# Kernel optimization log

Measured on AMD Instinct MI355X. Metric: run time of the kernel, lower is better.

Reference implementation:

```python
import jax, jax.numpy as jnp
import numpy as np

B, S, T = 4, 512, 512
V, D, F, H, DK, N = 32000, 512, 2048, 8, 64, 6
PAD = 0

# sinusoidal positional encoding table, matching the torch source exactly
_pos = np.arange(max(S, T))[:, None]
_i = np.arange(D // 2)[None, :]
_ang = _pos / (10000.0 ** (2 * _i / D))
_pe = np.empty((max(S, T), D), dtype=np.float32)
_pe[:, 0::2] = np.sin(_ang)
_pe[:, 1::2] = np.cos(_ang)
PE = jnp.asarray(_pe)


def setup_inputs() -> dict:
    key = jax.random.key(0)
    ks = iter(jax.random.split(key, 64))
    s = 0.02
    w = lambda shape: jax.random.normal(next(ks), shape, jnp.float32) * s
    inp = {
        'src': jax.random.randint(next(ks), (B, S), 0, V, jnp.int32),
        'trg': jax.random.randint(next(ks), (B, T), 0, V, jnp.int32),
        'emb_src': w((V, D)).at[PAD].set(0.0),
        'emb_trg': w((V, D)).at[PAD].set(0.0),
        # encoder stacks (leading axis = layer)
        'enc_wq': w((N, D, H * DK)), 'enc_wk': w((N, D, H * DK)),
        'enc_wv': w((N, D, H * DK)), 'enc_wo': w((N, H * DK, D)),
        'enc_ln1_g': jnp.ones((N, D)), 'enc_ln1_b': jnp.zeros((N, D)),
        'enc_w1': w((N, D, F)), 'enc_b1': jnp.zeros((N, F)),
        'enc_w2': w((N, F, D)), 'enc_b2': jnp.zeros((N, D)),
        'enc_ln2_g': jnp.ones((N, D)), 'enc_ln2_b': jnp.zeros((N, D)),
        # decoder stacks
        'dec_wq': w((N, D, H * DK)), 'dec_wk': w((N, D, H * DK)),
        'dec_wv': w((N, D, H * DK)), 'dec_wo': w((N, H * DK, D)),
        'dec_ln1_g': jnp.ones((N, D)), 'dec_ln1_b': jnp.zeros((N, D)),
        'dec_cq': w((N, D, H * DK)), 'dec_ck': w((N, D, H * DK)),
        'dec_cv': w((N, D, H * DK)), 'dec_co': w((N, H * DK, D)),
        'dec_ln2_g': jnp.ones((N, D)), 'dec_ln2_b': jnp.zeros((N, D)),
        'dec_w1': w((N, D, F)), 'dec_b1': jnp.zeros((N, F)),
        'dec_w2': w((N, F, D)), 'dec_b2': jnp.zeros((N, D)),
        'dec_ln3_g': jnp.ones((N, D)), 'dec_ln3_b': jnp.zeros((N, D)),
        'proj': w((D, V)),
    }
    return inp


def _ln(x, g, b, eps=1e-5):
    m = x.mean(-1, keepdims=True)
    v = ((x - m) ** 2).mean(-1, keepdims=True)
    return (x - m) * jax.lax.rsqrt(v + eps) * g + b


def _mha(xq, xkv, wq, wk, wv, wo, mask):
    b, lq, _ = xq.shape
    lk = xkv.shape[1]
    q = (xq @ wq).reshape(b, lq, H, DK).transpose(0, 2, 1, 3)   # bhqd
    k = (xkv @ wk).reshape(b, lk, H, DK).transpose(0, 2, 1, 3)  # bhkd
    v = (xkv @ wv).reshape(b, lk, H, DK).transpose(0, 2, 1, 3)  # bhkd
    scores = jnp.einsum('bhqd,bhkd->bhqk', q, k)
    scores = jnp.where(mask, -jnp.inf, scores)
    attn = jax.nn.softmax(scores * (DK ** -0.5), axis=-1)
    out = jnp.einsum('bhqk,bhkd->bhqd', attn, v)
    out = out.transpose(0, 2, 1, 3).reshape(b, lq, H * DK)
    return out @ wo


def _ffn(x, w1, b1, w2, b2):
    return jax.nn.relu(x @ w1 + b1) @ w2 + b2


def reference(src, trg, emb_src, emb_trg,
              enc_wq, enc_wk, enc_wv, enc_wo, enc_ln1_g, enc_ln1_b,
              enc_w1, enc_b1, enc_w2, enc_b2, enc_ln2_g, enc_ln2_b,
              dec_wq, dec_wk, dec_wv, dec_wo, dec_ln1_g, dec_ln1_b,
              dec_cq, dec_ck, dec_cv, dec_co, dec_ln2_g, dec_ln2_b,
              dec_w1, dec_b1, dec_w2, dec_b2, dec_ln3_g, dec_ln3_b,
              proj):
    scale = D ** 0.5
    src_pad = (src == PAD)[:, None, None, :]                 # [B,1,1,S]
    trg_pad = (trg == PAD)[:, None, None, :]                 # [B,1,1,T]
    causal = jnp.triu(jnp.ones((T, T), bool), 1)[None, None]  # [1,1,T,T]
    trg_mask = trg_pad | causal

    # encoder (dropout = identity in eval)
    x = emb_src[src] * scale + PE[None, :S]

    def enc_step(h, p):
        wq, wk, wv, wo, g1, b1, w1, bb1, w2, bb2, g2, b2 = p
        h = _ln(h + _mha(h, h, wq, wk, wv, wo, src_pad), g1, b1)
        h = _ln(h + _ffn(h, w1, bb1, w2, bb2), g2, b2)
        return h, None

    x_enc, _ = jax.lax.scan(enc_step, x,
        (enc_wq, enc_wk, enc_wv, enc_wo, enc_ln1_g, enc_ln1_b,
         enc_w1, enc_b1, enc_w2, enc_b2, enc_ln2_g, enc_ln2_b))

    # decoder
    y = emb_trg[trg] * scale + PE[None, :T]

    def dec_step(h, p):
        (wq, wk, wv, wo, g1, b1, cq, ck, cv, co, g2, b2,
         w1, bb1, w2, bb2, g3, b3) = p
        h = _ln(h + _mha(h, h, wq, wk, wv, wo, trg_mask), g1, b1)
        h = _ln(h + _mha(h, x_enc, cq, ck, cv, co, src_pad), g2, b2)
        h = _ln(h + _ffn(h, w1, bb1, w2, bb2), g3, b3)
        return h, None

    y, _ = jax.lax.scan(dec_step, y,
        (dec_wq, dec_wk, dec_wv, dec_wo, dec_ln1_g, dec_ln1_b,
         dec_cq, dec_ck, dec_cv, dec_co, dec_ln2_g, dec_ln2_b,
         dec_w1, dec_b1, dec_w2, dec_b2, dec_ln3_g, dec_ln3_b))

    return y @ proj  # [B, T, trg_vocab]
```

## Files before the change

### kernel.cpp

```cpp
#include <hip/hip_runtime.h>
#include <math.h>

#define BBATCH 4
#define SS 512
#define DDIM 512
#define FFN 2048
#define NHEAD 8
#define DHEAD 64
#define NL 6
#define NVOC 32000
#define MTOK (BBATCH*SS)
#define PAD_ID 0

typedef unsigned short u16;
typedef __attribute__((ext_vector_type(8))) short short8;
typedef __attribute__((ext_vector_type(4))) float f32x4;

__device__ __forceinline__ u16 f2bf(float f) {
    union { float f; unsigned u; } v; v.f = f;
    unsigned r = ((v.u >> 16) & 1u) + 0x7fffu;
    return (u16)((v.u + r) >> 16);
}

__device__ __forceinline__ void gload16(const u16* g, u16* l) {
    __builtin_amdgcn_global_load_lds(
        (const __attribute__((address_space(1))) void*)g,
        (__attribute__((address_space(3))) void*)l, 16, 0, 0);
}

template<int BM, int BN, int OUTBF, int RELU, int BIAS>
__device__ __forceinline__ void gemm_core(
    u16* __restrict__ AsB, u16* __restrict__ BsB,
    const u16* __restrict__ A, int lda,
    const u16* __restrict__ B, int ldb,
    void* __restrict__ Cv, int ldc,
    int row0, int col0, int K, const float* __restrict__ bias)
{
    const int tid  = threadIdx.x;
    const int lane = tid & 63;
    const int wid  = tid >> 6;
    const int wr   = wid >> 1, wc = wid & 1;
    constexpr int MF = BM / 32, NF = BN / 32, RA = BM / 64, RB = BN / 64;

    const u16* aSrc[RA]; int aOff[RA];
    #pragma unroll
    for (int r = 0; r < RA; r++) {
        int row = (tid >> 2) + r * 64;
        int slot = ((tid & 3) << 4) ^ ((row & 3) << 4);
        aSrc[r] = A + (size_t)(row0 + row) * lda + (slot >> 1);
        aOff[r] = r * 2048 + tid * 8;
    }
    const u16* bSrc[RB]; int bOff[RB];
    #pragma unroll
    for (int r = 0; r < RB; r++) {
        int row = (tid >> 2) + r * 64;
        int slot = ((tid & 3) << 4) ^ ((row & 3) << 4);
        bSrc[r] = B + (size_t)(col0 + row) * ldb + (slot >> 1);
        bOff[r] = r * 2048 + tid * 8;
    }

    f32x4 acc[MF][NF];
    const f32x4 zero = {0.f, 0.f, 0.f, 0.f};
    #pragma unroll
    for (int m = 0; m < MF; m++)
        #pragma unroll
        for (int n = 0; n < NF; n++) acc[m][n] = zero;

    const int nt = K / 32;
    #pragma unroll
    for (int r = 0; r < RA; r++) gload16(aSrc[r], AsB + aOff[r]);
    #pragma unroll
    for (int r = 0; r < RB; r++) gload16(bSrc[r], BsB + bOff[r]);
    __syncthreads();

    for (int t = 0; t < nt; t++) {
        const int cur = t & 1;
        if (t + 1 < nt) {
            u16* ad = AsB + (cur ^ 1) * (BM * 32);
            u16* bd = BsB + (cur ^ 1) * (BN * 32);
            #pragma unroll
            for (int r = 0; r < RA; r++) gload16(aSrc[r] + (t + 1) * 32, ad + aOff[r]);
            #pragma unroll
            for (int r = 0; r < RB; r++) gload16(bSrc[r] + (t + 1) * 32, bd + bOff[r]);
        }
        const u16* as = AsB + cur * (BM * 32);
        const u16* bs = BsB + cur * (BN * 32);
        short8 af[MF], bf[NF];
        #pragma unroll
        for (int m = 0; m < MF; m++) {
            int row = wr * (BM / 2) + m * 16 + (lane & 15);
            int slot = ((lane >> 4) << 4) ^ ((row & 3) << 4);
            af[m] = *(const short8*)&as[row * 32 + (slot >> 1)];
        }
        #pragma unroll
        for (int n = 0; n < NF; n++) {
            int row = wc * (BN / 2) + n * 16 + (lane & 15);
            int slot = ((lane >> 4) << 4) ^ ((row & 3) << 4);
            bf[n] = *(const short8*)&bs[row * 32 + (slot >> 1)];
        }
        #pragma unroll
        for (int m = 0; m < MF; m++)
            #pragma unroll
            for (int n = 0; n < NF; n++)
                acc[m][n] = __builtin_amdgcn_mfma_f32_16x16x32_bf16(af[m], bf[n], acc[m][n], 0, 0, 0);
        __syncthreads();
    }

    const int crow = row0 + wr * (BM / 2);
    const int ccol = col0 + wc * (BN / 2);
    #pragma unroll
    for (int m = 0; m < MF; m++) {
        #pragma unroll
        for (int n = 0; n < NF; n++) {
            int col = ccol + n * 16 + (lane & 15);
            float bv = BIAS ? bias[col] : 0.0f;
            #pragma unroll
            for (int i = 0; i < 4; i++) {
                int row = crow + m * 16 + ((lane >> 4) << 2) + i;
                float v = acc[m][n][i] + bv;
                if (RELU) v = fmaxf(v, 0.0f);
                if (OUTBF) ((u16*)Cv)[(size_t)row * ldc + col] = f2bf(v);
                else       ((float*)Cv)[(size_t)row * ldc + col] = v;
            }
        }
    }
}

template<int BM, int BN, int OUTBF, int RELU, int BIAS, int SWZ = 0>
__global__ __launch_bounds__(256) void mgemm(
    const u16* __restrict__ A, int lda, size_t aSb, size_t aSh,
    const u16* __restrict__ B, int ldb, size_t bSb, size_t bSh,
    void* __restrict__ Cv, int ldc, size_t cSb, size_t cSh,
    int K, const float* __restrict__ bias)
{
    __shared__ __align__(16) u16 As[2 * BM * 32];
    __shared__ __align__(16) u16 Bs[2 * BN * 32];
    int bx = blockIdx.x, by = blockIdx.y;
    if (SWZ) {
        int nwg = gridDim.x * gridDim.y;
        int lin = by * gridDim.x + bx;
        int cpx = nwg >> 3;
        int s = (lin & 7) * cpx + (lin >> 3);
        bx = s % gridDim.x; by = s / gridDim.x;
    }
    const int zb = blockIdx.z >> 3, zh = blockIdx.z & 7;
    const u16* Ab = A + (size_t)zb * aSb + (size_t)zh * aSh;
    const u16* Bb = B + (size_t)zb * bSb + (size_t)zh * bSh;
    void* Cb = OUTBF ? (void*)((u16*)Cv + (size_t)zb * cSb + (size_t)zh * cSh)
                     : (void*)((float*)Cv + (size_t)zb * cSb + (size_t)zh * cSh);
    gemm_core<BM, BN, OUTBF, RELU, BIAS>(As, Bs, Ab, lda, Bb, ldb, Cb, ldc,
                                          by * BM, bx * BN, K, bias);
}

template<int BM, int BN>
__global__ __launch_bounds__(256) void mgemm_dual(
    const u16* __restrict__ A1, int lda1, const u16* __restrict__ B1, int ldb1,
    u16* __restrict__ C1, int ldc1, int nx1, int nblk1,
    const u16* __restrict__ A2, int lda2, const u16* __restrict__ B2, int ldb2,
    u16* __restrict__ C2, int ldc2, int nx2,
    int K)
{
    __shared__ __align__(16) u16 As[2 * BM * 32];
    __shared__ __align__(16) u16 Bs[2 * BN * 32];
    int id = blockIdx.x;
    if (id < nblk1) {
        gemm_core<BM, BN, 1, 0, 0>(As, Bs, A1, lda1, B1, ldb1, C1, ldc1,
                                    (id / nx1) * BM, (id % nx1) * BN, K, nullptr);
    } else {
        id -= nblk1;
        gemm_core<BM, BN, 1, 0, 0>(As, Bs, A2, lda2, B2, ldb2, C2, ldc2,
                                    (id / nx2) * BM, (id % nx2) * BN, K, nullptr);
    }
}

template<int CAUSAL>
__global__ __launch_bounds__(256) void flash_attn(
    const u16* __restrict__ Qp, int ldq,
    const u16* __restrict__ Kp, int ldk,
    const u16* __restrict__ Vtp,
    u16* __restrict__ O,
    const int* __restrict__ ids)
{
    __shared__ __align__(16) u16 Kl[2][64 * 64];
    __shared__ __align__(16) u16 Vl[2][64 * 64];
    __shared__ __align__(16) u16 Pl[4][16 * 64];
    __shared__ float msk[SS];

    const int tid = threadIdx.x, lane = tid & 63, wid = tid >> 6;
    const int bh = blockIdx.y, b = bh >> 3, h = bh & 7;
    const int q0 = blockIdx.x * 64;

    for (int i = tid; i < SS; i += 256)
        msk[i] = (ids[b * SS + i] == PAD_ID) ? -1e30f : 0.0f;

    const int qloc = wid * 16 + (lane & 15);
    const u16* Qb = Qp + (size_t)(b * SS + q0 + qloc) * ldq + h * 64 + ((lane >> 4) * 8);
    short8 qf[2];
    qf[0] = *(const short8*)(Qb);
    qf[1] = *(const short8*)(Qb + 32);

    const u16* Kb = Kp + (size_t)b * SS * ldk + h * 64;
    const u16* Vb = Vtp + (size_t)(h * 64) * MTOK + b * SS;

    auto stage = [&](int buf, int kt) {
        int row = tid >> 3;
        int sl  = tid & 7;
        #pragma unroll
        for (int r = 0; r < 2; r++) {
            int rr = row + r * 32;
            int ls = sl ^ (rr & 7);
            gload16(Kb + (size_t)(kt * 64 + rr) * ldk + ls * 8, &Kl[buf][rr * 64 + sl * 8]);
            gload16(Vb + (size_t)rr * MTOK + kt * 64 + ls * 8, &Vl[buf][rr * 64 + sl * 8]);
        }
    };

    const int nt = CAUSAL ? (blockIdx.x + 1) : (SS / 64);
    stage(0, 0);
    __syncthreads();

    float m_i[4], l_i[4];
    f32x4 o_acc[4];
    const f32x4 zero = {0.f, 0.f, 0.f, 0.f};
    #pragma unroll
    for (int i = 0; i < 4; i++) { m_i[i] = -1e30f; l_i[i] = 0.0f; }
    #pragma unroll
    for (int n = 0; n < 4; n++) o_acc[n] = zero;

    for (int kt = 0; kt < nt; kt++) {
        int cur = kt & 1;
        if (kt + 1 < nt) stage(cur ^ 1, kt + 1);

        f32x4 s_acc[4];
        #pragma unroll
        for (int n = 0; n < 4; n++) s_acc[n] = zero;
        #pragma unroll
        for (int kk = 0; kk < 2; kk++) {
            #pragma unroll
            for (int n = 0; n < 4; n++) {
                int row = n * 16 + (lane & 15);
                int ls = (kk * 4 + (lane >> 4)) ^ (row & 7);
                short8 kf = *(const short8*)&Kl[cur][row * 64 + ls * 8];
                s_acc[n] = __builtin_amdgcn_mfma_f32_16x16x32_bf16(qf[kk], kf, s_acc[n], 0, 0, 0);
            }
        }

        float sv[4][4];
        #pragma unroll
        for (int n = 0; n < 4; n++) {
            int kg = kt * 64 + n * 16 + (lane & 15);
            float mk = msk[kg];
            #pragma unroll
            for (int i = 0; i < 4; i++) {
                float s = s_acc[n][i] * 0.125f + mk;
                if (CAUSAL) {
                    int qg = q0 + wid * 16 + ((lane >> 4) << 2) + i;
                    if (kg > qg) s = -1e30f;
                }
                sv[n][i] = s;
            }
        }
        float pm[4], mn[4], rs[4], ps[4];
        #pragma unroll
        for (int i = 0; i < 4; i++)
            pm[i] = fmaxf(fmaxf(sv[0][i], sv[1][i]), fmaxf(sv[2][i], sv[3][i]));
        #pragma unroll
        for (int i = 0; i < 4; i++) {
            #pragma unroll
            for (int msh = 1; msh <= 8; msh <<= 1)
                pm[i] = fmaxf(pm[i], __shfl_xor(pm[i], msh));
            mn[i] = fmaxf(m_i[i], pm[i]);
            rs[i] = __expf(m_i[i] - mn[i]);
            m_i[i] = mn[i];
        }
        float p[4][4];
        #pragma unroll
        for (int n = 0; n < 4; n++)
            #pragma unroll
            for (int i = 0; i < 4; i++)
                p[n][i] = (sv[n][i] < -1e29f) ? 0.0f : __expf(sv[n][i] - mn[i]);
        #pragma unroll
        for (int i = 0; i < 4; i++) {
            ps[i] = p[0][i] + p[1][i] + p[2][i] + p[3][i];
            #pragma unroll
            for (int msh = 1; msh <= 8; msh <<= 1)
                ps[i] += __shfl_xor(ps[i], msh);
            l_i[i] = l_i[i] * rs[i] + ps[i];
        }
        #pragma unroll
        for (int n = 0; n < 4; n++)
            #pragma unroll
            for (int i = 0; i < 4; i++)
                o_acc[n][i] *= rs[i];

        #pragma unroll
        for (int n = 0; n < 4; n++) {
            int k = n * 16 + (lane & 15);
            #pragma unroll
            for (int i = 0; i < 4; i++) {
                int q = ((lane >> 4) << 2) + i;
                Pl[wid][q * 64 + (((k >> 3) ^ (q & 7)) << 3) + (k & 7)] = f2bf(p[n][i]);
            }
        }
        asm volatile("s_waitcnt lgkmcnt(0)" ::: "memory");

        #pragma unroll
        for (int kk = 0; kk < 2; kk++) {
            int qrow = lane & 15;
            int lsp = (kk * 4 + (lane >> 4)) ^ (qrow & 7);
            short8 pa = *(const short8*)&Pl[wid][qrow * 64 + lsp * 8];
            #pragma unroll
            for (int nf = 0; nf < 4; nf++) {
                int row = nf * 16 + (lane & 15);
                int vs = (kk * 4 + (lane >> 4)) ^ (row & 7);
                short8 vf = *(const short8*)&Vl[cur][row * 64 + vs * 8];
                o_acc[nf] = __builtin_amdgcn_mfma_f32_16x16x32_bf16(pa, vf, o_acc[nf], 0, 0, 0);
            }
        }
        __syncthreads();
    }

    #pragma unroll
    for (int nf = 0; nf < 4; nf++) {
        int d = h * 64 + nf * 16 + (lane & 15);
        #pragma unroll
        for (int i = 0; i < 4; i++) {
            int qg = b * SS + q0 + wid * 16 + ((lane >> 4) << 2) + i;
            O[(size_t)qg * DDIM + d] = f2bf(o_acc[nf][i] / l_i[i]);
        }
    }
}

__device__ __forceinline__ void transp_core(const float* __restrict__ src, u16* __restrict__ dst,
                                            int N, int K, int n0, int k0)
{
    __shared__ u16 t[64][65];
    const int tid = threadIdx.x;
    #pragma unroll
    for (int i = 0; i < 16; i++) {
        int idx = tid + i * 256;
        int kr = idx >> 6, nc = idx & 63;
        t[kr][nc] = f2bf(src[(size_t)(k0 + kr) * N + n0 + nc]);
    }
    __syncthreads();
    #pragma unroll
    for (int i = 0; i < 16; i++) {
        int idx = tid + i * 256;
        int nr = idx >> 6, kc = idx & 63;
        dst[(size_t)(n0 + nr) * K + k0 + kc] = t[kc][nr];
    }
}

__global__ __launch_bounds__(256) void transp(const float* __restrict__ src, u16* __restrict__ dst,
                                              int N, int K, size_t sStride, size_t dStride)
{
    transp_core(src + (size_t)blockIdx.z * sStride, dst + (size_t)blockIdx.z * dStride,
                N, K, blockIdx.x * 64, blockIdx.y * 64);
}

#define OFF_QK 0u
#define OFF_WV 524288u
#define OFF_WO 786432u
#define OFF_CQ 1048576u
#define OFF_CK 1310720u
#define OFF_CV 1572864u
#define OFF_CO 1835008u
#define OFF_W1 2097152u
#define OFF_W2 3145728u
#define WBLK   4194304u
#define M2CNT  262144u
#define MF1CNT 1048576u

__global__ __launch_bounds__(256) void transpW(
    const float* p0, const float* p1, const float* p2, const float* p3,
    const float* p4, const float* p5, const float* p6, const float* p7,
    const float* p8, const float* p9, const float* p10, const float* p11,
    u16* __restrict__ wreg)
{
    int z = blockIdx.z;
    int w = z % 12, l = z / 12;
    const float* ptrs[12] = {p0,p1,p2,p3,p4,p5,p6,p7,p8,p9,p10,p11};
    const float* src = ptrs[w] + (size_t)l * M2CNT;
    u16* dst = wreg + (w < 4 ? (size_t)l * WBLK + (size_t)w * M2CNT
                             : (size_t)(NL + l) * WBLK + (size_t)(w - 4) * M2CNT);
    transp_core(src, dst, 512, 512, blockIdx.x * 64, blockIdx.y * 64);
}

__global__ __launch_bounds__(256) void transpF1(const float* __restrict__ e,
                                                const float* __restrict__ d, u16* __restrict__ wreg)
{
    int z = blockIdx.z; int l = z % NL, w = z / NL;
    const float* src = (w ? d : e) + (size_t)l * MF1CNT;
    u16* dst = wreg + (size_t)(w * NL + l) * WBLK + OFF_W1;
    transp_core(src, dst, 2048, 512, blockIdx.x * 64, blockIdx.y * 64);
}

__global__ __launch_bounds__(256) void transpF2(const float* __restrict__ e,
                                                const float* __restrict__ d, u16* __restrict__ wreg)
{
    int z = blockIdx.z; int l = z % NL, w = z / NL;
    const float* src = (w ? d : e) + (size_t)l * MF1CNT;
    u16* dst = wreg + (size_t)(w * NL + l) * WBLK + OFF_W2;
    transp_core(src, dst, 512, 2048, blockIdx.x * 64, blockIdx.y * 64);
}

__global__ void pe_kernel(float* __restrict__ PEt)
{
    int pos = blockIdx.x, d = threadIdx.x;
    int i = d >> 1;
    double freq = exp(-(2.0 * (double)i / (double)DDIM) * log(10000.0));
    double ang = (double)pos * freq;
    PEt[pos * DDIM + d] = (float)((d & 1) ? cos(ang) : sin(ang));
}

__global__ void embed_kernel(const int* __restrict__ ids, const float* __restrict__ emb,
                             const float* __restrict__ PEt,
                             float* __restrict__ out, u16* __restrict__ outb)
{
    int tok = blockIdx.x;
    int d = threadIdx.x;
    int pos = tok & (SS - 1);
    int id = ids[tok];
    float val = emb[(size_t)id * DDIM + d] * 22.62741699796952f + PEt[pos * DDIM + d];
    out[(size_t)tok * DDIM + d] = val;
    outb[(size_t)tok * DDIM + d] = f2bf(val);
}

__global__ __launch_bounds__(256) void add_ln_kernel(float* __restrict__ x,
    const float* __restrict__ addv, const float* __restrict__ g,
    const float* __restrict__ bta, u16* __restrict__ xb)
{
    int row = blockIdx.x;
    int tid = threadIdx.x;
    size_t base = (size_t)row * DDIM;
    __shared__ float sbuf[4];

    float v0 = x[base + tid]       + addv[base + tid];
    float v1 = x[base + tid + 256] + addv[base + tid + 256];

    float s = v0 + v1;
    #pragma unroll
    for (int o = 32; o > 0; o >>= 1) s += __shfl_down(s, o);
    if ((tid & 63) == 0) sbuf[tid >> 6] = s;
    __syncthreads();
    float mean = (sbuf[0] + sbuf[1] + sbuf[2] + sbuf[3]) * (1.0f / DDIM);
    __syncthreads();

    float d0 = v0 - mean, d1 = v1 - mean;
    float ss = d0 * d0 + d1 * d1;
    #pragma unroll
    for (int o = 32; o > 0; o >>= 1) ss += __shfl_down(ss, o);
    if ((tid & 63) == 0) sbuf[tid >> 6] = ss;
    __syncthreads();
    float var = (sbuf[0] + sbuf[1] + sbuf[2] + sbuf[3]) * (1.0f / DDIM);
    float inv = rsqrtf(var + 1e-5f);

    float o0 = d0 * inv * g[tid]       + bta[tid];
    float o1 = d1 * inv * g[tid + 256] + bta[tid + 256];
    x[base + tid] = o0;
    x[base + tid + 256] = o1;
    xb[base + tid] = f2bf(o0);
    xb[base + tid + 256] = f2bf(o1);
}

extern "C" void kernel_launch(void* const* d_in, const int* in_sizes, int n_in,
                              void* d_out, int out_size, void* d_ws, size_t ws_size,
                              hipStream_t stream)
{
    (void)in_sizes; (void)n_in; (void)out_size;

    const int*   src      = (const int*)  d_in[0];
    const int*   trg      = (const int*)  d_in[1];
    const float* emb_src  = (const float*)d_in[2];
    const float* emb_trg  = (const float*)d_in[3];
    const float* enc_wq   = (const float*)d_in[4];
    const float* enc_wk   = (const float*)d_in[5];
    const float* enc_wv   = (const float*)d_in[6];
    const float* enc_wo   = (const float*)d_in[7];
    const float* enc_ln1g = (const float*)d_in[8];
    const float* enc_ln1b = (const float*)d_in[9];
    const float* enc_w1   = (const float*)d_in[10];
    const float* enc_b1   = (const float*)d_in[11];
    const float* enc_w2   = (const float*)d_in[12];
    const float* enc_b2   = (const float*)d_in[13];
    const float* enc_ln2g = (const float*)d_in[14];
    const float* enc_ln2b = (const float*)d_in[15];
    const float* dec_wq   = (const float*)d_in[16];
    const float* dec_wk   = (const float*)d_in[17];
    const float* dec_wv   = (const float*)d_in[18];
    const float* dec_wo   = (const float*)d_in[19];
    const float* dec_ln1g = (const float*)d_in[20];
    const float* dec_ln1b = (const float*)d_in[21];
    const float* dec_cq   = (const float*)d_in[22];
    const float* dec_ck   = (const float*)d_in[23];
    const float* dec_cv   = (const float*)d_in[24];
    const float* dec_co   = (const float*)d_in[25];
    const float* dec_ln2g = (const float*)d_in[26];
    const float* dec_ln2b = (const float*)d_in[27];
    const float* dec_w1   = (const float*)d_in[28];
    const float* dec_b1   = (const float*)d_in[29];
    const float* dec_w2   = (const float*)d_in[30];
    const float* dec_b2   = (const float*)d_in[31];
    const float* dec_ln3g = (const float*)d_in[32];
    const float* dec_ln3b = (const float*)d_in[33];
    const float* proj     = (const float*)d_in[34];

    float* OUT = (float*)d_out;
    char* base = (char*)d_ws;

    const size_t MSZ = (size_t)MTOK * DDIM;
    size_t off = 0;
    auto carve = [&](size_t bytes) { char* p = base + off; off += (bytes + 255) & ~(size_t)255; return p; };

    float* X      = (float*)carve(MSZ * 4);
    float* Yb     = (float*)carve(MSZ * 4);
    float* T1     = (float*)carve(MSZ * 4);
    u16*   Xb     = (u16*)  carve(MSZ * 2);
    u16*   Ybf    = (u16*)  carve(MSZ * 2);
    u16*   QKb    = (u16*)  carve((size_t)MTOK * 1024 * 2);
    u16*   Vt     = (u16*)  carve((size_t)512 * MTOK * 2);
    u16*   CTX    = (u16*)  carve(MSZ * 2);
    u16*   HFF    = (u16*)  carve((size_t)MTOK * FFN * 2);
    u16*   Kcr    = (u16*)  carve((size_t)NL * MTOK * 512 * 2);
    u16*   Vtc    = (u16*)  carve((size_t)NL * 512 * MTOK * 2);
    u16*   projT  = (u16*)  carve((size_t)NVOC * 512 * 2);
    float* PEt    = (float*)carve((size_t)SS * DDIM * 4);

    const size_t WFULL_B = (size_t)12 * WBLK * 2;
    bool full = (ws_size >= off + WFULL_B);
    u16* Wreg = (u16*)carve(full ? WFULL_B : (size_t)WBLK * 2);

    auto T = [&](const float* s, u16* d, int Kd, int Nd, size_t ss, size_t ds, int L) {
        transp<<<dim3(Nd / 64, Kd / 64, L), 256, 0, stream>>>(s, d, Nd, Kd, ss, ds);
    };

    pe_kernel<<<SS, DDIM, 0, stream>>>(PEt);
    T(proj, projT, 512, NVOC, 0, 0, 1);
    if (full) {
        transpW<<<dim3(8, 8, 12 * NL), 256, 0, stream>>>(
            enc_wq, enc_wk, enc_wv, enc_wo,
            dec_wq, dec_wk, dec_wv, dec_wo,
            dec_cq, dec_ck, dec_cv, dec_co, Wreg);
        transpF1<<<dim3(32, 8, 2 * NL), 256, 0, stream>>>(enc_w1, dec_w1, Wreg);
        transpF2<<<dim3(8, 32, 2 * NL), 256, 0, stream>>>(enc_w2, dec_w2, Wreg);
    }

    auto self_attn = [&](const u16* xsrc, const u16* wb, const int* mask_ids, int causal) {
        mgemm_dual<64, 128><<<dim3(384), 256, 0, stream>>>(
            xsrc, 512, wb + OFF_QK, 512, QKb, 1024, 8, 256,
            wb + OFF_WV, 512, xsrc, 512, Vt, MTOK, 16,
            512);
        if (causal)
            flash_attn<1><<<dim3(8, 32), 256, 0, stream>>>(QKb, 1024, QKb + 512, 1024, Vt, CTX, mask_ids);
        else
            flash_attn<0><<<dim3(8, 32), 256, 0, stream>>>(QKb, 1024, QKb + 512, 1024, Vt, CTX, mask_ids);
        mgemm<64, 64, 0, 0, 0><<<dim3(8, 32, 1), 256, 0, stream>>>(
            CTX, 512, 0, 0, wb + OFF_WO, 512, 0, 0, T1, 512, 0, 0, 512, nullptr);
    };

    const size_t M2 = M2CNT, MF1 = MF1CNT;

    embed_kernel<<<MTOK, DDIM, 0, stream>>>(src, emb_src, PEt, X, Xb);
    for (int l = 0; l < NL; l++) {
        u16* wb;
        if (full) wb = Wreg + (size_t)l * WBLK;
        else {
            wb = Wreg;
            T(enc_wq + l * M2,  wb + OFF_QK,          512, 512,  0, 0, 1);
            T(enc_wk + l * M2,  wb + OFF_QK + M2,     512, 512,  0, 0, 1);
            T(enc_wv + l * M2,  wb + OFF_WV,          512, 512,  0, 0, 1);
            T(enc_wo + l * M2,  wb + OFF_WO,          512, 512,  0, 0, 1);
            T(enc_w1 + l * MF1, wb + OFF_W1,          512, 2048, 0, 0, 1);
            T(enc_w2 + l * MF1, wb + OFF_W2,          2048, 512, 0, 0, 1);
        }
        self_attn(Xb, wb, src, 0);
        add_ln_kernel<<<MTOK, 256, 0, stream>>>(X, T1, enc_ln1g + l * DDIM, enc_ln1b + l * DDIM, Xb);
        mgemm<128, 128, 1, 1, 1><<<dim3(16, 16, 1), 256, 0, stream>>>(
            Xb, 512, 0, 0, wb + OFF_W1, 512, 0, 0, HFF, FFN, 0, 0, 512, enc_b1 + l * FFN);
        mgemm<64, 64, 0, 0, 1><<<dim3(8, 32, 1), 256, 0, stream>>>(
            HFF, FFN, 0, 0, wb + OFF_W2, FFN, 0, 0, T1, 512, 0, 0, FFN, enc_b2 + l * DDIM);
        add_ln_kernel<<<MTOK, 256, 0, stream>>>(X, T1, enc_ln2g + l * DDIM, enc_ln2b + l * DDIM, Xb);
    }

    if (full) {
        u16* Wd = Wreg + (size_t)NL * WBLK;
        mgemm<128, 128, 1, 0, 0><<<dim3(4, 16, NL), 256, 0, stream>>>(
            Xb, 512, 0, 0, Wd + OFF_CK, 512, 0, WBLK, Kcr, 512, 0, (size_t)MTOK * 512, 512, nullptr);
        mgemm<128, 128, 1, 0, 0><<<dim3(16, 4, NL), 256, 0, stream>>>(
            Wd + OFF_CV, 512, 0, WBLK, Xb, 512, 0, 0, Vtc, MTOK, 0, (size_t)512 * MTOK, 512, nullptr);
    }

    embed_kernel<<<MTOK, DDIM, 0, stream>>>(trg, emb_trg, PEt, Yb, Ybf);
    for (int l = 0; l < NL; l++) {
        u16* wb;
        if (full) wb = Wreg + (size_t)(NL + l) * WBLK;
        else {
            wb = Wreg;
            T(dec_wq + l * M2,  wb + OFF_QK,          512, 512,  0, 0, 1);
            T(dec_wk + l * M2,  wb + OFF_QK + M2,     512, 512,  0, 0, 1);
            T(dec_wv + l * M2,  wb + OFF_WV,          512, 512,  0, 0, 1);
            T(dec_wo + l * M2,  wb + OFF_WO,          512, 512,  0, 0, 1);
            T(dec_cq + l * M2,  wb + OFF_CQ,          512, 512,  0, 0, 1);
            T(dec_ck + l * M2,  wb + OFF_CK,          512, 512,  0, 0, 1);
            T(dec_cv + l * M2,  wb + OFF_CV,          512, 512,  0, 0, 1);
            T(dec_co + l * M2,  wb + OFF_CO,          512, 512,  0, 0, 1);
            T(dec_w1 + l * MF1, wb + OFF_W1,          512, 2048, 0, 0, 1);
            T(dec_w2 + l * MF1, wb + OFF_W2,          2048, 512, 0, 0, 1);
            mgemm<128, 128, 1, 0, 0><<<dim3(4, 16, 1), 256, 0, stream>>>(
                Xb, 512, 0, 0, wb + OFF_CK, 512, 0, 0, Kcr + (size_t)l * MTOK * 512, 512, 0, 0, 512, nullptr);
            mgemm<128, 128, 1, 0, 0><<<dim3(16, 4, 1), 256, 0, stream>>>(
                wb + OFF_CV, 512, 0, 0, Xb, 512, 0, 0, Vtc + (size_t)l * 512 * MTOK, MTOK, 0, 0, 512, nullptr);
        }
        self_attn(Ybf, wb, trg, 1);
        add_ln_kernel<<<MTOK, 256, 0, stream>>>(Yb, T1, dec_ln1g + l * DDIM, dec_ln1b + l * DDIM, Ybf);
        mgemm<64, 64, 1, 0, 0><<<dim3(8, 32, 1), 256, 0, stream>>>(
            Ybf, 512, 0, 0, wb + OFF_CQ, 512, 0, 0, QKb, 1024, 0, 0, 512, nullptr);
        flash_attn<0><<<dim3(8, 32), 256, 0, stream>>>(
            QKb, 1024, Kcr + (size_t)l * MTOK * 512, 512, Vtc + (size_t)l * 512 * MTOK, CTX, src);
        mgemm<64, 64, 0, 0, 0><<<dim3(8, 32, 1), 256, 0, stream>>>(
            CTX, 512, 0, 0, wb + OFF_CO, 512, 0, 0, T1, 512, 0, 0, 512, nullptr);
        add_ln_kernel<<<MTOK, 256, 0, stream>>>(Yb, T1, dec_ln2g + l * DDIM, dec_ln2b + l * DDIM, Ybf);
        mgemm<128, 128, 1, 1, 1><<<dim3(16, 16, 1), 256, 0, stream>>>(
            Ybf, 512, 0, 0, wb + OFF_W1, 512, 0, 0, HFF, FFN, 0, 0, 512, dec_b1 + l * FFN);
        mgemm<64, 64, 0, 0, 1><<<dim3(8, 32, 1), 256, 0, stream>>>(
            HFF, FFN, 0, 0, wb + OFF_W2, FFN, 0, 0, T1, 512, 0, 0, FFN, dec_b2 + l * DDIM);
        add_ln_kernel<<<MTOK, 256, 0, stream>>>(Yb, T1, dec_ln3g + l * DDIM, dec_ln3b + l * DDIM, Ybf);
    }

    mgemm<128, 128, 0, 0, 0, 1><<<dim3(NVOC / 128, 16, 1), 256, 0, stream>>>(
        Ybf, 512, 0, 0, projT, 512, 0, 0, OUT, NVOC, 0, 0, 512, nullptr);
}
```

Baseline: 1.587 ms.

## Split-K FFN down-projection, larger attention tiles, MFMA priority hints, merged embeddings

Several independent changes land together. The FFN second GEMM becomes a 4-way split-K batched GEMM writing partial sums, and a new add+LayerNorm kernel reduces those partials and adds the bias. Flash attention moves to 128-query blocks with 512 threads, and the QK/V dual GEMM uses 128x128 tiles. s_setprio hints wrap the MFMA loops, and the two embedding launches are merged into one. The goal is fewer launches, better occupancy on the K=2048 GEMM and more K/V reuse per block, at the cost of extra partial-sum memory traffic and fewer attention blocks.

```diff
diff --git a/kernel.cpp b/kernel.cpp
--- a/kernel.cpp
+++ b/kernel.cpp
@@ -11,6 +11,7 @@
 #define NVOC 32000
 #define MTOK (BBATCH*SS)
 #define PAD_ID 0
+#define MSZE ((size_t)MTOK * DDIM)
 
 typedef unsigned short u16;
 typedef __attribute__((ext_vector_type(8))) short short8;
@@ -98,11 +99,13 @@
             int slot = ((lane >> 4) << 4) ^ ((row & 3) << 4);
             bf[n] = *(const short8*)&bs[row * 32 + (slot >> 1)];
         }
+        __builtin_amdgcn_s_setprio(1);
         #pragma unroll
         for (int m = 0; m < MF; m++)
             #pragma unroll
             for (int n = 0; n < NF; n++)
                 acc[m][n] = __builtin_amdgcn_mfma_f32_16x16x32_bf16(af[m], bf[n], acc[m][n], 0, 0, 0);
+        __builtin_amdgcn_s_setprio(0);
         __syncthreads();
     }
 
@@ -174,7 +177,7 @@
 }
 
 template<int CAUSAL>
-__global__ __launch_bounds__(256) void flash_attn(
+__global__ __launch_bounds__(512) void flash_attn(
     const u16* __restrict__ Qp, int ldq,
     const u16* __restrict__ Kp, int ldk,
     const u16* __restrict__ Vtp,
@@ -183,14 +186,14 @@
 {
     __shared__ __align__(16) u16 Kl[2][64 * 64];
     __shared__ __align__(16) u16 Vl[2][64 * 64];
-    __shared__ __align__(16) u16 Pl[4][16 * 64];
+    __shared__ __align__(16) u16 Pl[8][16 * 64];
     __shared__ float msk[SS];
 
     const int tid = threadIdx.x, lane = tid & 63, wid = tid >> 6;
     const int bh = blockIdx.y, b = bh >> 3, h = bh & 7;
-    const int q0 = blockIdx.x * 64;
-
-    for (int i = tid; i < SS; i += 256)
+    const int q0 = blockIdx.x * 128;
+
+    for (int i = tid; i < SS; i += 512)
         msk[i] = (ids[b * SS + i] == PAD_ID) ? -1e30f : 0.0f;
 
     const int qloc = wid * 16 + (lane & 15);
@@ -205,16 +208,12 @@
     auto stage = [&](int buf, int kt) {
         int row = tid >> 3;
         int sl  = tid & 7;
-        #pragma unroll
-        for (int r = 0; r < 2; r++) {
-            int rr = row + r * 32;
-            int ls = sl ^ (rr & 7);
-            gload16(Kb + (size_t)(kt * 64 + rr) * ldk + ls * 8, &Kl[buf][rr * 64 + sl * 8]);
-            gload16(Vb + (size_t)rr * MTOK + kt * 64 + ls * 8, &Vl[buf][rr * 64 + sl * 8]);
-        }
+        int ls = sl ^ (row & 7);
+        gload16(Kb + (size_t)(kt * 64 + row) * ldk + ls * 8, &Kl[buf][row * 64 + sl * 8]);
+        gload16(Vb + (size_t)row * MTOK + kt * 64 + ls * 8, &Vl[buf][row * 64 + sl * 8]);
     };
 
-    const int nt = CAUSAL ? (blockIdx.x + 1) : (SS / 64);
+    const int nt = CAUSAL ? (2 * blockIdx.x + 2) : (SS / 64);
     stage(0, 0);
     __syncthreads();
 
@@ -233,6 +232,7 @@
         f32x4 s_acc[4];
         #pragma unroll
         for (int n = 0; n < 4; n++) s_acc[n] = zero;
+        __builtin_amdgcn_s_setprio(1);
         #pragma unroll
         for (int kk = 0; kk < 2; kk++) {
             #pragma unroll
@@ -243,6 +243,7 @@
                 s_acc[n] = __builtin_amdgcn_mfma_f32_16x16x32_bf16(qf[kk], kf, s_acc[n], 0, 0, 0);
             }
         }
+        __builtin_amdgcn_s_setprio(0);
 
         float sv[4][4];
         #pragma unroll
@@ -302,7 +303,9 @@
             }
         }
         asm volatile("s_waitcnt lgkmcnt(0)" ::: "memory");
-
+        __builtin_amdgcn_sched_barrier(0);
+
+        __builtin_amdgcn_s_setprio(1);
         #pragma unroll
         for (int kk = 0; kk < 2; kk++) {
             int qrow = lane & 15;
@@ -316,6 +319,7 @@
                 o_acc[nf] = __builtin_amdgcn_mfma_f32_16x16x32_bf16(pa, vf, o_acc[nf], 0, 0, 0);
             }
         }
+        __builtin_amdgcn_s_setprio(0);
         __syncthreads();
     }
 
@@ -412,17 +416,22 @@
     PEt[pos * DDIM + d] = (float)((d & 1) ? cos(ang) : sin(ang));
 }
 
-__global__ void embed_kernel(const int* __restrict__ ids, const float* __restrict__ emb,
+__global__ void embed_kernel(const int* __restrict__ src, const int* __restrict__ trg,
+                             const float* __restrict__ es, const float* __restrict__ et,
                              const float* __restrict__ PEt,
-                             float* __restrict__ out, u16* __restrict__ outb)
-{
-    int tok = blockIdx.x;
+                             float* __restrict__ X, u16* __restrict__ Xb,
+                             float* __restrict__ Y, u16* __restrict__ Ybf)
+{
+    int gtok = blockIdx.x;
     int d = threadIdx.x;
+    bool dec = gtok >= MTOK;
+    int tok = dec ? gtok - MTOK : gtok;
     int pos = tok & (SS - 1);
-    int id = ids[tok];
+    int id = (dec ? trg : src)[tok];
+    const float* emb = dec ? et : es;
     float val = emb[(size_t)id * DDIM + d] * 22.62741699796952f + PEt[pos * DDIM + d];
-    out[(size_t)tok * DDIM + d] = val;
-    outb[(size_t)tok * DDIM + d] = f2bf(val);
+    (dec ? Y : X)[(size_t)tok * DDIM + d] = val;
+    (dec ? Ybf : Xb)[(size_t)tok * DDIM + d] = f2bf(val);
 }
 
 __global__ __launch_bounds__(256) void add_ln_kernel(float* __restrict__ x,
@@ -436,6 +445,48 @@
 
     float v0 = x[base + tid]       + addv[base + tid];
     float v1 = x[base + tid + 256] + addv[base + tid + 256];
+
+    float s = v0 + v1;
+    #pragma unroll
+    for (int o = 32; o > 0; o >>= 1) s += __shfl_down(s, o);
+    if ((tid & 63) == 0) sbuf[tid >> 6] = s;
+    __syncthreads();
+    float mean = (sbuf[0] + sbuf[1] + sbuf[2] + sbuf[3]) * (1.0f / DDIM);
+    __syncthreads();
+
+    float d0 = v0 - mean, d1 = v1 - mean;
+    float ss = d0 * d0 + d1 * d1;
+    #pragma unroll
+    for (int o = 32; o > 0; o >>= 1) ss += __shfl_down(ss, o);
+    if ((tid & 63) == 0) sbuf[tid >> 6] = ss;
+    __syncthreads();
+    float var = (sbuf[0] + sbuf[1] + sbuf[2] + sbuf[3]) * (1.0f / DDIM);
+    float inv = rsqrtf(var + 1e-5f);
+
+    float o0 = d0 * inv * g[tid]       + bta[tid];
+    float o1 = d1 * inv * g[tid + 256] + bta[tid + 256];
+    x[base + tid] = o0;
+    x[base + tid + 256] = o1;
+    xb[base + tid] = f2bf(o0);
+    xb[base + tid + 256] = f2bf(o1);
+}
+
+__global__ __launch_bounds__(256) void add_ln_red(float* __restrict__ x,
+    const float* __restrict__ part, const float* __restrict__ bias,
+    const float* __restrict__ g, const float* __restrict__ bta, u16* __restrict__ xb)
+{
+    int row = blockIdx.x;
+    int tid = threadIdx.x;
+    size_t base = (size_t)row * DDIM;
+    __shared__ float sbuf[4];
+
+    float v0 = x[base + tid]       + bias[tid];
+    float v1 = x[base + tid + 256] + bias[tid + 256];
+    #pragma unroll
+    for (int s4 = 0; s4 < 4; s4++) {
+        v0 += part[s4 * MSZE + base + tid];
+        v1 += part[s4 * MSZE + base + tid + 256];
+    }
 
     float s = v0 + v1;
     #pragma unroll
@@ -507,23 +558,23 @@
     float* OUT = (float*)d_out;
     char* base = (char*)d_ws;
 
-    const size_t MSZ = (size_t)MTOK * DDIM;
     size_t off = 0;
     auto carve = [&](size_t bytes) { char* p = base + off; off += (bytes + 255) & ~(size_t)255; return p; };
 
-    float* X      = (float*)carve(MSZ * 4);
-    float* Yb     = (float*)carve(MSZ * 4);
-    float* T1     = (float*)carve(MSZ * 4);
-    u16*   Xb     = (u16*)  carve(MSZ * 2);
-    u16*   Ybf    = (u16*)  carve(MSZ * 2);
+    float* X      = (float*)carve(MSZE * 4);
+    float* Yb     = (float*)carve(MSZE * 4);
+    float* T1     = (float*)carve(MSZE * 4);
+    u16*   Xb     = (u16*)  carve(MSZE * 2);
+    u16*   Ybf    = (u16*)  carve(MSZE * 2);
     u16*   QKb    = (u16*)  carve((size_t)MTOK * 1024 * 2);
     u16*   Vt     = (u16*)  carve((size_t)512 * MTOK * 2);
-    u16*   CTX    = (u16*)  carve(MSZ * 2);
+    u16*   CTX    = (u16*)  carve(MSZE * 2);
     u16*   HFF    = (u16*)  carve((size_t)MTOK * FFN * 2);
     u16*   Kcr    = (u16*)  carve((size_t)NL * MTOK * 512 * 2);
     u16*   Vtc    = (u16*)  carve((size_t)NL * 512 * MTOK * 2);
     u16*   projT  = (u16*)  carve((size_t)NVOC * 512 * 2);
     float* PEt    = (float*)carve((size_t)SS * DDIM * 4);
+    float* Tp4    = (float*)carve((size_t)4 * MSZE * 4);
 
     const size_t WFULL_B = (size_t)12 * WBLK * 2;
     bool full = (ws_size >= off + WFULL_B);
@@ -543,23 +594,31 @@
         transpF1<<<dim3(32, 8, 2 * NL), 256, 0, stream>>>(enc_w1, dec_w1, Wreg);
         transpF2<<<dim3(8, 32, 2 * NL), 256, 0, stream>>>(enc_w2, dec_w2, Wreg);
     }
+    embed_kernel<<<2 * MTOK, DDIM, 0, stream>>>(src, trg, emb_src, emb_trg, PEt, X, Xb, Yb, Ybf);
 
     auto self_attn = [&](const u16* xsrc, const u16* wb, const int* mask_ids, int causal) {
-        mgemm_dual<64, 128><<<dim3(384), 256, 0, stream>>>(
-            xsrc, 512, wb + OFF_QK, 512, QKb, 1024, 8, 256,
+        mgemm_dual<128, 128><<<dim3(192), 256, 0, stream>>>(
+            xsrc, 512, wb + OFF_QK, 512, QKb, 1024, 8, 128,
             wb + OFF_WV, 512, xsrc, 512, Vt, MTOK, 16,
             512);
         if (causal)
-            flash_attn<1><<<dim3(8, 32), 256, 0, stream>>>(QKb, 1024, QKb + 512, 1024, Vt, CTX, mask_ids);
+            flash_attn<1><<<dim3(4, 32), 512, 0, stream>>>(QKb, 1024, QKb + 512, 1024, Vt, CTX, mask_ids);
         else
-            flash_attn<0><<<dim3(8, 32), 256, 0, stream>>>(QKb, 1024, QKb + 512, 1024, Vt, CTX, mask_ids);
+            flash_attn<0><<<dim3(4, 32), 512, 0, stream>>>(QKb, 1024, QKb + 512, 1024, Vt, CTX, mask_ids);
         mgemm<64, 64, 0, 0, 0><<<dim3(8, 32, 1), 256, 0, stream>>>(
             CTX, 512, 0, 0, wb + OFF_WO, 512, 0, 0, T1, 512, 0, 0, 512, nullptr);
     };
 
+    auto ffn = [&](const u16* xsrc, const u16* wb, const float* b1) {
+        mgemm<128, 128, 1, 1, 1><<<dim3(16, 16, 1), 256, 0, stream>>>(
+            xsrc, 512, 0, 0, wb + OFF_W1, 512, 0, 0, HFF, FFN, 0, 0, 512, b1);
+        mgemm<128, 128, 0, 0, 0><<<dim3(4, 16, 4), 256, 0, stream>>>(
+            HFF, 2048, 0, 512, wb + OFF_W2, 2048, 0, 512,
+            Tp4, 512, 0, MSZE, 512, nullptr);
+    };
+
     const size_t M2 = M2CNT, MF1 = MF1CNT;
 
-    embed_kernel<<<MTOK, DDIM, 0, stream>>>(src, emb_src, PEt, X, Xb);
     for (int l = 0; l < NL; l++) {
         u16* wb;
         if (full) wb = Wreg + (size_t)l * WBLK;
@@ -574,11 +633,9 @@
         }
         self_attn(Xb, wb, src, 0);
         add_ln_kernel<<<MTOK, 256, 0, stream>>>(X, T1, enc_ln1g + l * DDIM, enc_ln1b + l * DDIM, Xb);
-        mgemm<128, 128, 1, 1, 1><<<dim3(16, 16, 1), 256, 0, stream>>>(
-            Xb, 512, 0, 0, wb + OFF_W1, 512, 0, 0, HFF, FFN, 0, 0, 512, enc_b1 + l * FFN);
-        mgemm<64, 64, 0, 0, 1><<<dim3(8, 32, 1), 256, 0, stream>>>(
-            HFF, FFN, 0, 0, wb + OFF_W2, FFN, 0, 0, T1, 512, 0, 0, FFN, enc_b2 + l * DDIM);
-        add_ln_kernel<<<MTOK, 256, 0, stream>>>(X, T1, enc_ln2g + l * DDIM, enc_ln2b + l * DDIM, Xb);
+        ffn(Xb, wb, enc_b1 + l * FFN);
+        add_ln_red<<<MTOK, 256, 0, stream>>>(X, Tp4, enc_b2 + l * DDIM,
+                                             enc_ln2g + l * DDIM, enc_ln2b + l * DDIM, Xb);
     }
 
     if (full) {
@@ -589,7 +646,6 @@
             Wd + OFF_CV, 512, 0, WBLK, Xb, 512, 0, 0, Vtc, MTOK, 0, (size_t)512 * MTOK, 512, nullptr);
     }
 
-    embed_kernel<<<MTOK, DDIM, 0, stream>>>(trg, emb_trg, PEt, Yb, Ybf);
     for (int l = 0; l < NL; l++) {
         u16* wb;
         if (full) wb = Wreg + (size_t)(NL + l) * WBLK;
@@ -614,16 +670,14 @@
         add_ln_kernel<<<MTOK, 256, 0, stream>>>(Yb, T1, dec_ln1g + l * DDIM, dec_ln1b + l * DDIM, Ybf);
         mgemm<64, 64, 1, 0, 0><<<dim3(8, 32, 1), 256, 0, stream>>>(
             Ybf, 512, 0, 0, wb + OFF_CQ, 512, 0, 0, QKb, 1024, 0, 0, 512, nullptr);
-        flash_attn<0><<<dim3(8, 32), 256, 0, stream>>>(
+        flash_attn<0><<<dim3(4, 32), 512, 0, stream>>>(
             QKb, 1024, Kcr + (size_t)l * MTOK * 512, 512, Vtc + (size_t)l * 512 * MTOK, CTX, src);
         mgemm<64, 64, 0, 0, 0><<<dim3(8, 32, 1), 256, 0, stream>>>(
             CTX, 512, 0, 0, wb + OFF_CO, 512, 0, 0, T1, 512, 0, 0, 512, nullptr);
         add_ln_kernel<<<MTOK, 256, 0, stream>>>(Yb, T1, dec_ln2g + l * DDIM, dec_ln2b + l * DDIM, Ybf);
-        mgemm<128, 128, 1, 1, 1><<<dim3(16, 16, 1), 256, 0, stream>>>(
-            Ybf, 512, 0, 0, wb + OFF_W1, 512, 0, 0, HFF, FFN, 0, 0, 512, dec_b1 + l * FFN);
-        mgemm<64, 64, 0, 0, 1><<<dim3(8, 32, 1), 256, 0, stream>>>(
-            HFF, FFN, 0, 0, wb + OFF_W2, FFN, 0, 0, T1, 512, 0, 0, FFN, dec_b2 + l * DDIM);
-        add_ln_kernel<<<MTOK, 256, 0, stream>>>(Yb, T1, dec_ln3g + l * DDIM, dec_ln3b + l * DDIM, Ybf);
+        ffn(Ybf, wb, dec_b1 + l * FFN);
+        add_ln_red<<<MTOK, 256, 0, stream>>>(Yb, Tp4, dec_b2 + l * DDIM,
+                                             dec_ln3g + l * DDIM, dec_ln3b + l * DDIM, Ybf);
     }
 
     mgemm<128, 128, 0, 0, 0, 1><<<dim3(NVOC / 128, 16, 1), 256, 0, stream>>>(
```

New measurement: 1.573 ms. About the same (-0.8%).
